# Optimization experiments

Hardware: AMD Instinct MI355X
Metric: run time of the kernel (lower is better)

## Reference

```python
import jax, jax.numpy as jnp
import numpy as np

B, S, H = 2, 2048, 1024
NUM_HEAD = 16
HEAD = H // NUM_HEAD
NEG = -10000000000.0


def setup_inputs() -> dict:
    key = jax.random.key(0)
    ks = jax.random.split(key, 10)
    scale = 1.0 / np.sqrt(H)
    return {
        "query": jax.random.normal(ks[0], (B, S, H), jnp.float32),
        "key": jax.random.normal(ks[1], (B, S, H), jnp.float32),
        "value": jax.random.normal(ks[2], (B, S, H), jnp.float32),
        "mask": jax.random.randint(ks[3], (B, S), 0, 2, jnp.int32),
        "Wq": jax.random.normal(ks[4], (H, H), jnp.float32) * scale,
        "bq": jnp.zeros((H,), jnp.float32),
        "Wk": jax.random.normal(ks[5], (H, H), jnp.float32) * scale,
        "bk": jnp.zeros((H,), jnp.float32),
        "Wv": jax.random.normal(ks[6], (H, H), jnp.float32) * scale,
        "bv": jnp.zeros((H,), jnp.float32),
    }


def reference(query, key, value, mask, Wq, bq, Wk, bk, Wv, bv):
    b, s, h = query.shape
    # Linear projections (torch Linear: x @ W.T + b), split into heads -> [b, nh, s, hd]
    def proj(x, W, bias):
        y = x @ W.T + bias
        return y.reshape(b, s, NUM_HEAD, HEAD).transpose(0, 2, 1, 3)

    q = proj(query, Wq, bq)
    k = proj(key, Wk, bk)
    v = proj(value, Wv, bv)

    # NOTE: original module has NO 1/sqrt(head_dim) scaling -- faithful.
    attn_score = jnp.einsum("bhqd,bhkd->bhqk", q, k)  # [b, nh, s, s]
    # key-padding mask bias: 0 where mask==1, -1e10 where mask==0, broadcast over query dim
    bias_add = jnp.where(mask[:, None, None, :] == 0, NEG, 0.0).astype(attn_score.dtype)
    attn_score = attn_score + bias_add
    attn_ratio = jax.nn.softmax(attn_score, axis=-1)
    out = jnp.einsum("bhqk,bhkd->bhqd", attn_ratio, v)  # [b, nh, s, hd]
    out = out.transpose(0, 2, 1, 3).reshape(b, s, h)
    # Dropout is identity in eval mode; output_linear is defined but never used in forward.
    return out
```

## Files before the change

kernel.cpp:

```cpp
#include <hip/hip_runtime.h>

#define BATCH 2
#define S_LEN 2048
#define HDIM  1024
#define NHEAD 16
#define HD    64
#define NEGBIAS -1e10f

typedef __attribute__((ext_vector_type(8))) _Float16 half8;
typedef __attribute__((ext_vector_type(4))) float   f32x4;

__global__ __launch_bounds__(256) void cvt_w(
    const float* __restrict__ Wq, const float* __restrict__ Wk,
    const float* __restrict__ Wv, _Float16* __restrict__ Wf)
{
    const int z = blockIdx.y;
    const float* src = (z == 0) ? Wq : (z == 1) ? Wk : Wv;
    _Float16* dst = Wf + (size_t)z * (HDIM * HDIM);
    size_t i = ((size_t)blockIdx.x * 256 + threadIdx.x) * 8;
    float4 a0 = *(const float4*)(src + i);
    float4 a1 = *(const float4*)(src + i + 4);
    half8 v;
    v[0] = (_Float16)a0.x; v[1] = (_Float16)a0.y;
    v[2] = (_Float16)a0.z; v[3] = (_Float16)a0.w;
    v[4] = (_Float16)a1.x; v[5] = (_Float16)a1.y;
    v[6] = (_Float16)a1.z; v[7] = (_Float16)a1.w;
    *(half8*)(dst + i) = v;
}

__global__ __launch_bounds__(256) void proj_gemm_f16(
    const float* __restrict__ Xq, const float* __restrict__ Xk,
    const float* __restrict__ Xv, const _Float16* __restrict__ Wf,
    const float* __restrict__ bq, const float* __restrict__ bk,
    const float* __restrict__ bv,
    _Float16* __restrict__ Qb, _Float16* __restrict__ Kb, _Float16* __restrict__ Vtb)
{
    const int z = blockIdx.z;
    const float* X    = (z == 0) ? Xq : (z == 1) ? Xk : Xv;
    const float* bias = (z == 0) ? bq : (z == 1) ? bk : bv;
    const _Float16* Wz = Wf + (size_t)z * (HDIM * HDIM);
    _Float16* Y       = (z == 0) ? Qb : (z == 1) ? Kb : Vtb;

    const int n0 = blockIdx.x * 128;
    const int m0 = blockIdx.y * 128;

    __shared__ __align__(16) _Float16 As[128][40];
    __shared__ __align__(16) _Float16 Bs[128][40];

    const int t    = threadIdx.x;
    const int w    = t >> 6;
    const int lane = t & 63;
    const int quad = lane >> 4;
    const int lc   = lane & 15;
    const int wm   = (w >> 1) * 64;
    const int wn   = (w & 1) * 64;

    const f32x4 fzero = {0.f, 0.f, 0.f, 0.f};
    f32x4 acc[4][4];
#pragma unroll
    for (int i = 0; i < 4; i++)
#pragma unroll
        for (int j = 0; j < 4; j++) acc[i][j] = fzero;

    const int srow = t >> 2;
    const int sc   = t & 3;

    for (int k0 = 0; k0 < HDIM; k0 += 32) {
#pragma unroll
        for (int half = 0; half < 2; half++) {
            int row = srow + half * 64;
            {
                const float* g = X + (size_t)(m0 + row) * HDIM + k0 + sc * 8;
                float4 a0 = *(const float4*)g;
                float4 a1 = *(const float4*)(g + 4);
                half8 v;
                v[0] = (_Float16)a0.x; v[1] = (_Float16)a0.y;
                v[2] = (_Float16)a0.z; v[3] = (_Float16)a0.w;
                v[4] = (_Float16)a1.x; v[5] = (_Float16)a1.y;
                v[6] = (_Float16)a1.z; v[7] = (_Float16)a1.w;
                *(half8*)&As[row][sc * 8] = v;
            }
            *(half8*)&Bs[row][sc * 8] =
                *(const half8*)(Wz + (size_t)(n0 + row) * HDIM + k0 + sc * 8);
        }
        __syncthreads();

        half8 af[4], bf[4];
#pragma unroll
        for (int mt = 0; mt < 4; mt++)
            af[mt] = *(const half8*)&As[wm + mt * 16 + lc][quad * 8];
#pragma unroll
        for (int nt = 0; nt < 4; nt++)
            bf[nt] = *(const half8*)&Bs[wn + nt * 16 + lc][quad * 8];
#pragma unroll
        for (int mt = 0; mt < 4; mt++)
#pragma unroll
            for (int nt = 0; nt < 4; nt++)
                acc[mt][nt] = __builtin_amdgcn_mfma_f32_16x16x32_f16(
                    af[mt], bf[nt], acc[mt][nt], 0, 0, 0);
        __syncthreads();
    }

#pragma unroll
    for (int nt = 0; nt < 4; nt++) {
        const int n = n0 + wn + nt * 16 + lc;
        const float bv_ = bias[n];
        const int h = n >> 6, d = n & 63;
#pragma unroll
        for (int mt = 0; mt < 4; mt++) {
#pragma unroll
            for (int r = 0; r < 4; r++) {
                const int m = m0 + wm + mt * 16 + quad * 4 + r;
                const int b = m >> 11, s = m & (S_LEN - 1);
                const int bh = b * NHEAD + h;
                _Float16 val = (_Float16)(acc[mt][nt][r] + bv_);
                if (z == 2)
                    Y[((size_t)bh * HD + d) * S_LEN + s] = val;
                else
                    Y[((size_t)bh * S_LEN + s) * HD + d] = val;
            }
        }
    }
}

__global__ __launch_bounds__(256) void flash_attn_mfma(
    const _Float16* __restrict__ Qb, const _Float16* __restrict__ Kb,
    const _Float16* __restrict__ Vtb, const int* __restrict__ mask,
    float* __restrict__ out)
{
    const int qt = blockIdx.x & 31;
    const int bh = blockIdx.x >> 5;
    const int b  = bh >> 4;
    const int h  = bh & (NHEAD - 1);

    __shared__ __align__(16) _Float16 Ks [64][72];
    __shared__ __align__(16) _Float16 Vts[64][72];
    __shared__ __align__(16) _Float16 Ps [4][16][72];
    __shared__ float biasS[64];

    const int t    = threadIdx.x;
    const int w    = t >> 6;
    const int lane = t & 63;
    const int quad = lane >> 4;
    const int lc   = lane & 15;

    const _Float16* Kbase = Kb  + (size_t)bh * S_LEN * HD;
    const _Float16* Vbase = Vtb + (size_t)bh * HD * S_LEN;

    const int qrow = qt * 64 + w * 16 + lc;
    half8 qf[2];
#pragma unroll
    for (int s = 0; s < 2; s++)
        qf[s] = *(const half8*)(Qb + ((size_t)bh * S_LEN + qrow) * HD + s * 32 + quad * 8);

    const f32x4 fzero = {0.f, 0.f, 0.f, 0.f};
    f32x4 o[4];
#pragma unroll
    for (int nt = 0; nt < 4; nt++) o[nt] = fzero;
    float mrun = -3.0e38f;
    float lrun = 0.f;

    for (int kt = 0; kt < S_LEN; kt += 64) {
#pragma unroll
        for (int i = 0; i < 2; i++) {
            int c  = t + 256 * i;
            int rr = c >> 3;
            int cc = (c & 7) * 8;
            *(half8*)&Ks[rr][cc] =
                *(const half8*)(Kbase + (size_t)(kt + rr) * HD + cc);
            *(half8*)&Vts[rr][cc] =
                *(const half8*)(Vbase + (size_t)rr * S_LEN + kt + cc);
        }
        if (t < 64) biasS[t] = mask[b * S_LEN + kt + t] ? 0.f : NEGBIAS;
        __syncthreads();

        f32x4 scf[4];
#pragma unroll
        for (int tt = 0; tt < 4; tt++) scf[tt] = fzero;
#pragma unroll
        for (int s = 0; s < 2; s++) {
#pragma unroll
            for (int tt = 0; tt < 4; tt++) {
                half8 kf = *(const half8*)&Ks[tt * 16 + lc][s * 32 + quad * 8];
                scf[tt] = __builtin_amdgcn_mfma_f32_16x16x32_f16(kf, qf[s], scf[tt], 0, 0, 0);
            }
        }

#pragma unroll
        for (int tt = 0; tt < 4; tt++) {
            float4 b4 = *(const float4*)&biasS[tt * 16 + quad * 4];
            scf[tt][0] += b4.x; scf[tt][1] += b4.y;
            scf[tt][2] += b4.z; scf[tt][3] += b4.w;
        }

        float mx = scf[0][0];
#pragma unroll
        for (int tt = 0; tt < 4; tt++)
#pragma unroll
            for (int r = 0; r < 4; r++) mx = fmaxf(mx, scf[tt][r]);
        mx = fmaxf(mx, __shfl_xor(mx, 16));
        mx = fmaxf(mx, __shfl_xor(mx, 32));

        float mn = fmaxf(mrun, mx);
        float al = __expf(mrun - mn);
        float ls = 0.f;
#pragma unroll
        for (int tt = 0; tt < 4; tt++)
#pragma unroll
            for (int r = 0; r < 4; r++) {
                float p = __expf(scf[tt][r] - mn);
                scf[tt][r] = p;
                ls += p;
            }
        ls += __shfl_xor(ls, 16);
        ls += __shfl_xor(ls, 32);
        lrun = lrun * al + ls;
        mrun = mn;
#pragma unroll
        for (int nt = 0; nt < 4; nt++) {
            o[nt][0] *= al; o[nt][1] *= al; o[nt][2] *= al; o[nt][3] *= al;
        }

#pragma unroll
        for (int tt = 0; tt < 4; tt++)
#pragma unroll
            for (int r = 0; r < 4; r++)
                Ps[w][lc][tt * 16 + quad * 4 + r] = (_Float16)scf[tt][r];

#pragma unroll
        for (int s = 0; s < 2; s++) {
            half8 pf = *(const half8*)&Ps[w][lc][s * 32 + quad * 8];
#pragma unroll
            for (int nt = 0; nt < 4; nt++) {
                half8 vf = *(const half8*)&Vts[nt * 16 + lc][s * 32 + quad * 8];
                o[nt] = __builtin_amdgcn_mfma_f32_16x16x32_f16(vf, pf, o[nt], 0, 0, 0);
            }
        }
        __syncthreads();
    }

    const float inv = 1.f / lrun;
    const size_t rowb = ((size_t)b * S_LEN + qrow) * HDIM + h * HD;
#pragma unroll
    for (int nt = 0; nt < 4; nt++) {
        float4 v;
        v.x = o[nt][0] * inv; v.y = o[nt][1] * inv;
        v.z = o[nt][2] * inv; v.w = o[nt][3] * inv;
        *(float4*)&out[rowb + nt * 16 + quad * 4] = v;
    }
}

extern "C" void kernel_launch(void* const* d_in, const int* in_sizes, int n_in,
                              void* d_out, int out_size, void* d_ws, size_t ws_size,
                              hipStream_t stream) {
    const float* query = (const float*)d_in[0];
    const float* key   = (const float*)d_in[1];
    const float* value = (const float*)d_in[2];
    const int*   mask  = (const int*)  d_in[3];
    const float* Wq    = (const float*)d_in[4];
    const float* bq    = (const float*)d_in[5];
    const float* Wk    = (const float*)d_in[6];
    const float* bk    = (const float*)d_in[7];
    const float* Wv    = (const float*)d_in[8];
    const float* bv    = (const float*)d_in[9];
    float* out = (float*)d_out;

    const size_t nElem = (size_t)BATCH * S_LEN * HDIM;
    const size_t wElem = (size_t)HDIM * HDIM;
    if (ws_size < (3 * nElem + 3 * wElem) * sizeof(_Float16)) return;
    _Float16* Qb  = (_Float16*)d_ws;
    _Float16* Kb  = Qb + nElem;
    _Float16* Vtb = Kb + nElem;
    _Float16* Wf  = Vtb + nElem;

    dim3 gcvt(wElem / (256 * 8), 3);
    cvt_w<<<gcvt, 256, 0, stream>>>(Wq, Wk, Wv, Wf);

    dim3 gproj(HDIM / 128, (BATCH * S_LEN) / 128, 3);
    proj_gemm_f16<<<gproj, 256, 0, stream>>>(query, key, value, Wf,
                                             bq, bk, bv, Qb, Kb, Vtb);

    flash_attn_mfma<<<BATCH * NHEAD * (S_LEN / 64), 256, 0, stream>>>(
        Qb, Kb, Vtb, mask, out);
}
```

Before: 252.1 us.

## Process two 16-row query groups per warp in flash attention

```diff
diff --git a/kernel.cpp b/kernel.cpp
--- a/kernel.cpp
+++ b/kernel.cpp
@@ -8,6 +8,7 @@
 #define NEGBIAS -1e10f
 
 typedef __attribute__((ext_vector_type(8))) _Float16 half8;
+typedef __attribute__((ext_vector_type(4))) _Float16 half4;
 typedef __attribute__((ext_vector_type(4))) float   f32x4;
 
 __global__ __launch_bounds__(256) void cvt_w(
@@ -128,14 +129,14 @@
     const _Float16* __restrict__ Vtb, const int* __restrict__ mask,
     float* __restrict__ out)
 {
-    const int qt = blockIdx.x & 31;
-    const int bh = blockIdx.x >> 5;
+    const int qt = blockIdx.x & 15;
+    const int bh = blockIdx.x >> 4;
     const int b  = bh >> 4;
     const int h  = bh & (NHEAD - 1);
 
     __shared__ __align__(16) _Float16 Ks [64][72];
     __shared__ __align__(16) _Float16 Vts[64][72];
-    __shared__ __align__(16) _Float16 Ps [4][16][72];
+    __shared__ __align__(16) _Float16 Ps [4][32][72];
     __shared__ float biasS[64];
 
     const int t    = threadIdx.x;
@@ -147,18 +148,24 @@
     const _Float16* Kbase = Kb  + (size_t)bh * S_LEN * HD;
     const _Float16* Vbase = Vtb + (size_t)bh * HD * S_LEN;
 
-    const int qrow = qt * 64 + w * 16 + lc;
-    half8 qf[2];
-#pragma unroll
-    for (int s = 0; s < 2; s++)
-        qf[s] = *(const half8*)(Qb + ((size_t)bh * S_LEN + qrow) * HD + s * 32 + quad * 8);
+    half8 qf[2][2];
+#pragma unroll
+    for (int qg = 0; qg < 2; qg++) {
+        const int qrow = qt * 128 + w * 32 + qg * 16 + lc;
+#pragma unroll
+        for (int s = 0; s < 2; s++)
+            qf[qg][s] = *(const half8*)(Qb + ((size_t)bh * S_LEN + qrow) * HD
+                                        + s * 32 + quad * 8);
+    }
 
     const f32x4 fzero = {0.f, 0.f, 0.f, 0.f};
-    f32x4 o[4];
-#pragma unroll
-    for (int nt = 0; nt < 4; nt++) o[nt] = fzero;
-    float mrun = -3.0e38f;
-    float lrun = 0.f;
+    f32x4 o[2][4];
+#pragma unroll
+    for (int qg = 0; qg < 2; qg++)
+#pragma unroll
+        for (int nt = 0; nt < 4; nt++) o[qg][nt] = fzero;
+    float mrun[2] = {-3.0e38f, -3.0e38f};
+    float lrun[2] = {0.f, 0.f};
 
     for (int kt = 0; kt < S_LEN; kt += 64) {
 #pragma unroll
@@ -174,79 +181,97 @@
         if (t < 64) biasS[t] = mask[b * S_LEN + kt + t] ? 0.f : NEGBIAS;
         __syncthreads();
 
-        f32x4 scf[4];
-#pragma unroll
-        for (int tt = 0; tt < 4; tt++) scf[tt] = fzero;
+        f32x4 scf[2][4];
+#pragma unroll
+        for (int qg = 0; qg < 2; qg++)
+#pragma unroll
+            for (int tt = 0; tt < 4; tt++) scf[qg][tt] = fzero;
 #pragma unroll
         for (int s = 0; s < 2; s++) {
 #pragma unroll
             for (int tt = 0; tt < 4; tt++) {
                 half8 kf = *(const half8*)&Ks[tt * 16 + lc][s * 32 + quad * 8];
-                scf[tt] = __builtin_amdgcn_mfma_f32_16x16x32_f16(kf, qf[s], scf[tt], 0, 0, 0);
+                scf[0][tt] = __builtin_amdgcn_mfma_f32_16x16x32_f16(kf, qf[0][s], scf[0][tt], 0, 0, 0);
+                scf[1][tt] = __builtin_amdgcn_mfma_f32_16x16x32_f16(kf, qf[1][s], scf[1][tt], 0, 0, 0);
             }
         }
 
 #pragma unroll
         for (int tt = 0; tt < 4; tt++) {
             float4 b4 = *(const float4*)&biasS[tt * 16 + quad * 4];
-            scf[tt][0] += b4.x; scf[tt][1] += b4.y;
-            scf[tt][2] += b4.z; scf[tt][3] += b4.w;
-        }
-
-        float mx = scf[0][0];
-#pragma unroll
-        for (int tt = 0; tt < 4; tt++)
-#pragma unroll
-            for (int r = 0; r < 4; r++) mx = fmaxf(mx, scf[tt][r]);
-        mx = fmaxf(mx, __shfl_xor(mx, 16));
-        mx = fmaxf(mx, __shfl_xor(mx, 32));
-
-        float mn = fmaxf(mrun, mx);
-        float al = __expf(mrun - mn);
-        float ls = 0.f;
-#pragma unroll
-        for (int tt = 0; tt < 4; tt++)
-#pragma unroll
-            for (int r = 0; r < 4; r++) {
-                float p = __expf(scf[tt][r] - mn);
-                scf[tt][r] = p;
-                ls += p;
-            }
-        ls += __shfl_xor(ls, 16);
-        ls += __shfl_xor(ls, 32);
-        lrun = lrun * al + ls;
-        mrun = mn;
-#pragma unroll
-        for (int nt = 0; nt < 4; nt++) {
-            o[nt][0] *= al; o[nt][1] *= al; o[nt][2] *= al; o[nt][3] *= al;
-        }
-
-#pragma unroll
-        for (int tt = 0; tt < 4; tt++)
-#pragma unroll
-            for (int r = 0; r < 4; r++)
-                Ps[w][lc][tt * 16 + quad * 4 + r] = (_Float16)scf[tt][r];
+#pragma unroll
+            for (int qg = 0; qg < 2; qg++) {
+                scf[qg][tt][0] += b4.x; scf[qg][tt][1] += b4.y;
+                scf[qg][tt][2] += b4.z; scf[qg][tt][3] += b4.w;
+            }
+        }
+
+#pragma unroll
+        for (int qg = 0; qg < 2; qg++) {
+            float mx = scf[qg][0][0];
+#pragma unroll
+            for (int tt = 0; tt < 4; tt++)
+#pragma unroll
+                for (int r = 0; r < 4; r++) mx = fmaxf(mx, scf[qg][tt][r]);
+            mx = fmaxf(mx, __shfl_xor(mx, 16));
+            mx = fmaxf(mx, __shfl_xor(mx, 32));
+
+            float mn = fmaxf(mrun[qg], mx);
+            float al = __expf(mrun[qg] - mn);
+            float ls = 0.f;
+#pragma unroll
+            for (int tt = 0; tt < 4; tt++)
+#pragma unroll
+                for (int r = 0; r < 4; r++) {
+                    float p = __expf(scf[qg][tt][r] - mn);
+                    scf[qg][tt][r] = p;
+                    ls += p;
+                }
+            ls += __shfl_xor(ls, 16);
+            ls += __shfl_xor(ls, 32);
+            lrun[qg] = lrun[qg] * al + ls;
+            mrun[qg] = mn;
+#pragma unroll
+            for (int nt = 0; nt < 4; nt++) {
+                o[qg][nt][0] *= al; o[qg][nt][1] *= al;
+                o[qg][nt][2] *= al; o[qg][nt][3] *= al;
+            }
+
+#pragma unroll
+            for (int tt = 0; tt < 4; tt++) {
+                half4 pk;
+                pk[0] = (_Float16)scf[qg][tt][0]; pk[1] = (_Float16)scf[qg][tt][1];
+                pk[2] = (_Float16)scf[qg][tt][2]; pk[3] = (_Float16)scf[qg][tt][3];
+                *(half4*)&Ps[w][qg * 16 + lc][tt * 16 + quad * 4] = pk;
+            }
+        }
 
 #pragma unroll
         for (int s = 0; s < 2; s++) {
-            half8 pf = *(const half8*)&Ps[w][lc][s * 32 + quad * 8];
+            half8 pf0 = *(const half8*)&Ps[w][lc]     [s * 32 + quad * 8];
+            half8 pf1 = *(const half8*)&Ps[w][16 + lc][s * 32 + quad * 8];
 #pragma unroll
             for (int nt = 0; nt < 4; nt++) {
                 half8 vf = *(const half8*)&Vts[nt * 16 + lc][s * 32 + quad * 8];
-                o[nt] = __builtin_amdgcn_mfma_f32_16x16x32_f16(vf, pf, o[nt], 0, 0, 0);
+                o[0][nt] = __builtin_amdgcn_mfma_f32_16x16x32_f16(vf, pf0, o[0][nt], 0, 0, 0);
+                o[1][nt] = __builtin_amdgcn_mfma_f32_16x16x32_f16(vf, pf1, o[1][nt], 0, 0, 0);
             }
         }
         __syncthreads();
     }
 
-    const float inv = 1.f / lrun;
-    const size_t rowb = ((size_t)b * S_LEN + qrow) * HDIM + h * HD;
-#pragma unroll
-    for (int nt = 0; nt < 4; nt++) {
-        float4 v;
-        v.x = o[nt][0] * inv; v.y = o[nt][1] * inv;
-        v.z = o[nt][2] * inv; v.w = o[nt][3] * inv;
-        *(float4*)&out[rowb + nt * 16 + quad * 4] = v;
+#pragma unroll
+    for (int qg = 0; qg < 2; qg++) {
+        const int qrow = qt * 128 + w * 32 + qg * 16 + lc;
+        const float inv = 1.f / lrun[qg];
+        const size_t rowb = ((size_t)b * S_LEN + qrow) * HDIM + h * HD;
+#pragma unroll
+        for (int nt = 0; nt < 4; nt++) {
+            float4 v;
+            v.x = o[qg][nt][0] * inv; v.y = o[qg][nt][1] * inv;
+            v.z = o[qg][nt][2] * inv; v.w = o[qg][nt][3] * inv;
+            *(float4*)&out[rowb + nt * 16 + quad * 4] = v;
+        }
     }
 }
 
@@ -280,6 +305,6 @@
     proj_gemm_f16<<<gproj, 256, 0, stream>>>(query, key, value, Wf,
                                              bq, bk, bv, Qb, Kb, Vtb);
 
-    flash_attn_mfma<<<BATCH * NHEAD * (S_LEN / 64), 256, 0, stream>>>(
+    flash_attn_mfma<<<BATCH * NHEAD * (S_LEN / 128), 256, 0, stream>>>(
         Qb, Kb, Vtb, mask, out);
 }
```

After: 246.6 us. 1.02x faster.
